# Kernel optimization log

Hardware: AMD Instinct MI355X
Metric: run time of the kernel (lower is better)

Reference implementation:

```python
import jax, jax.numpy as jnp
import numpy as np

B, L, D, P = 2, 2048, 768, 1152
I1, I2 = 2048, 3072
H, HD1, HD2 = 12, 64, 96
NC, NP, ND = 3, 6, 3
EPS, ROPE_BASE = 1e-5, 10000.0
STACK_KEYS = ('wq', 'wk', 'wv', 'wo', 'w1', 'w2', 'w3', 'ln1', 'ln2')


def rope_cache(seq_len, n_elem):
    theta = 1.0 / (ROPE_BASE ** (jnp.arange(0, n_elem, 2, dtype=jnp.float32) / n_elem))
    freqs = jnp.outer(jnp.arange(seq_len, dtype=jnp.float32), theta)
    emb = jnp.concatenate([freqs, freqs], axis=-1)  # [T, n_elem]
    return jnp.cos(emb), jnp.sin(emb)


def apply_rope(x, cos, sin):
    half = x.shape[-1] // 2
    x1, x2 = x[..., :half], x[..., half:]
    return x * cos[None, None] + jnp.concatenate([-x2, x1], axis=-1) * sin[None, None]


def rmsnorm(x, w):
    return x * jax.lax.rsqrt(jnp.mean(x * x, axis=-1, keepdims=True) + EPS) * w


def block(x, p, cos, sin):
    Bx, T, Dm = x.shape
    hd = Dm // H
    h = rmsnorm(x, p['ln1'])
    q = (h @ p['wq']).reshape(Bx, T, H, hd).transpose(0, 2, 1, 3)
    k = (h @ p['wk']).reshape(Bx, T, H, hd).transpose(0, 2, 1, 3)
    v = (h @ p['wv']).reshape(Bx, T, H, hd).transpose(0, 2, 1, 3)
    q, k = apply_rope(q, cos, sin), apply_rope(k, cos, sin)
    scores = jnp.einsum('bhqd,bhkd->bhqk', q, k) / jnp.sqrt(jnp.float32(hd))
    scores = jnp.where(jnp.tril(jnp.ones((T, T), dtype=bool)), scores, -jnp.inf)
    o = jnp.einsum('bhqk,bhkd->bhqd', jax.nn.softmax(scores, axis=-1), v)
    x = x + o.transpose(0, 2, 1, 3).reshape(Bx, T, Dm) @ p['wo']
    h = rmsnorm(x, p['ln2'])
    return x + (jax.nn.silu(h @ p['w1']) * (h @ p['w3'])) @ p['w2']


def stack(x, fl, pre, n_layers, cos, sin):
    for i in range(n_layers):
        p = {k: fl[pre + '_' + k][i] for k in STACK_KEYS}
        x = block(x, p, cos, sin)
    return x


def compressor_trunk(fl, cos, sin):
    h = stack(fl['x'], fl, 'comp', NC, cos, sin)
    h = rmsnorm(h, fl['comp_norm'])
    logits = (jax.nn.silu(h @ fl['router_w1'] + fl['router_b1']) @ fl['router_w2'] + fl['router_b2'])[..., 0]
    probs = jax.nn.sigmoid(logits)
    hard = (probs > 0.5).astype(h.dtype)
    bmask = (probs + jax.lax.stop_gradient(hard - probs)).at[:, 0].set(1.0)  # STE
    return h, bmask


def compute_S(fl):
    cos1, sin1 = rope_cache(fl['x'].shape[1], HD1)
    _, bmask = compressor_trunk(fl, cos1, sin1)
    return int(jnp.max(jnp.sum(bmask, axis=-1)))


def model_forward(fl, S):
    Lx = fl['x'].shape[1]
    cos1, sin1 = rope_cache(Lx, HD1)
    h, bmask = compressor_trunk(fl, cos1, sin1)
    bdet = jax.lax.stop_gradient(bmask)
    counts = jnp.sum(bdet, axis=-1).astype(jnp.int32)  # [B]
    cum = jnp.cumsum(bdet, axis=-1)
    assignment = (cum[:, None, :] == jnp.arange(1, S + 1, dtype=cum.dtype)[None, :, None]).astype(h.dtype)
    select = assignment * bmask[:, None, :]  # [B,S,L] one-hot select, grads via STE
    boundaries = jnp.argsort(1.0 - bdet, axis=-1)[:, :S]  # stable desc sort of 0/1 mask
    xc = jnp.einsum('bsl,bld->bsd', select, h) @ fl['up_w']  # ragged gather as GEMM (as original)
    cos2, sin2 = rope_cache(S, HD2)
    xp = rmsnorm(stack(xc, fl, 'proc', NP, cos2, sin2), fl['proc_norm']) @ fl['down_w']
    # decoder: broadcast each chunk embedding back over its positions
    valid = counts[:, None] > jnp.arange(S)[None, :]
    starts = jnp.where(valid[:, :, None], boundaries[:, :, None], Lx)  # [B,S,1]
    chunk_ids = jnp.sum(jnp.arange(Lx)[None, None, :] >= starts, axis=1) - 1  # [B,L]
    y = jnp.take_along_axis(xp, chunk_ids[..., None], axis=1) + h
    y = stack(y, fl, 'dec', ND, cos1, sin1)
    return rmsnorm(y, fl['dec_norm'])


def setup_inputs():
    ks = iter(jax.random.split(jax.random.key(0), 64))
    def w(*shape):
        return jax.random.normal(next(ks), shape, dtype=jnp.float32) * 0.02
    inp = {'x': jax.random.normal(next(ks), (B, L, D), dtype=jnp.float32)}
    for pre, n, d, it in (('comp', NC, D, I1), ('proc', NP, P, I2), ('dec', ND, D, I1)):
        for nm in ('wq', 'wk', 'wv', 'wo'):
            inp[pre + '_' + nm] = w(n, d, d)
        inp[pre + '_w1'], inp[pre + '_w3'], inp[pre + '_w2'] = w(n, d, it), w(n, d, it), w(n, it, d)
        inp[pre + '_ln1'] = jnp.ones((n, d), jnp.float32)
        inp[pre + '_ln2'] = jnp.ones((n, d), jnp.float32)
        inp[pre + '_norm'] = jnp.ones((d,), jnp.float32)
    inp['router_w1'], inp['router_b1'] = w(D, D), jnp.zeros((D,), jnp.float32)
    inp['router_w2'], inp['router_b2'] = w(D, 1), jnp.zeros((1,), jnp.float32)
    inp['up_w'], inp['down_w'] = w(D, P), w(P, D)
    return inp


def reference(x, comp_wq, comp_wk, comp_wv, comp_wo, comp_w1, comp_w2, comp_w3, comp_ln1, comp_ln2, comp_norm, router_w1, router_b1, router_w2, router_b2, up_w, down_w, proc_wq, proc_wk, proc_wv, proc_wo, proc_w1, proc_w2, proc_w3, proc_ln1, proc_ln2, proc_norm, dec_wq, dec_wk, dec_wv, dec_wo, dec_w1, dec_w2, dec_w3, dec_ln1, dec_ln2, dec_norm):
    fl = dict(locals())  # exactly the forward args
    S = compute_S(fl)  # data-dependent number of chunks (concrete, eager)
    return model_forward(fl, S)
```

## Files before the change

### kernel.cpp

```cpp
#include <hip/hip_runtime.h>
#include <cstdint>

static constexpr int LSEQ = 2048;
static constexpr int NHEAD = 12;

typedef unsigned short u16;
typedef __attribute__((ext_vector_type(8))) short bf16x8;
typedef __attribute__((ext_vector_type(8))) unsigned short u16x8;
typedef __attribute__((ext_vector_type(4))) float f32x4;

#define MFMA16 __builtin_amdgcn_mfma_f32_16x16x32_bf16

union U8cvt { u16 u[8]; bf16x8 v; u16x8 w; };

__device__ __forceinline__ float silu(float a) { return a / (1.f + __expf(-a)); }

__device__ __forceinline__ void splitf(float x, u16& h, u16& l) {
    uint32_t ux = __float_as_uint(x);
    uint32_t uh = (ux + 0x7fffu + ((ux >> 16) & 1u)) >> 16;
    float hf = __uint_as_float(uh << 16);
    float r = x - hf;
    uint32_t ur = __float_as_uint(r);
    uint32_t ul = (ur + 0x7fffu + ((ur >> 16) & 1u)) >> 16;
    h = (u16)uh; l = (u16)ul;
}

__device__ __forceinline__ void gld16(const void* g, void* l) {
    __builtin_amdgcn_global_load_lds((const __attribute__((address_space(1))) void*)g,
                                     (__attribute__((address_space(3))) void*)l, 16, 0, 0);
}

struct SplitEnt { const float* s0; const float* s1; const float* s2;
                  u16* dhi; u16* dlo; int K; int Nper; int nsrc; int bstart; };
struct SplitArgs { SplitEnt e[4]; int ne; };

__global__ __launch_bounds__(256)
void wsplit_k(SplitArgs a)
{
    const int blk = blockIdx.x;
    int ti = a.ne - 1;
    for (int i = 1; i < a.ne; ++i) if (blk < a.e[i].bstart) { ti = i - 1; break; }
    const SplitEnt E = a.e[ti];
    const int N = E.Nper * E.nsrc;
    const int u = (blk - E.bstart) * 256 + threadIdx.x;
    const int n = u % N, kb = u / N;
    const int which = n / E.Nper, col = n - which * E.Nper;
    const float* sp = (which == 0 ? E.s0 : which == 1 ? E.s1 : E.s2)
                      + (size_t)(kb * 8) * E.Nper + col;
    U8cvt hh, ll;
#pragma unroll
    for (int j = 0; j < 8; ++j) splitf(sp[(size_t)j * E.Nper], hh.u[j], ll.u[j]);
    *(u16x8*)(E.dhi + (size_t)u * 8) = hh.w;
    *(u16x8*)(E.dlo + (size_t)u * 8) = ll.w;
}

template<bool MASK>
__global__ __launch_bounds__(256)
void gemm_mfma_k(const u16* __restrict__ Ahi, const u16* __restrict__ Alo,
                 const u16* __restrict__ Bhi, const u16* __restrict__ Blo,
                 const float* __restrict__ Res, float* __restrict__ C,
                 int N, int K, const int* __restrict__ dS)
{
    const int n0 = blockIdx.x * 128;
    const int m0 = blockIdx.y * 128;
    int S = 1 << 30;
    if (MASK) { S = *dS; if ((m0 & (LSEQ - 1)) >= S) return; }

    __shared__ u16 sm[32768];
    u16* sAhi = sm;
    u16* sAlo = sm + 8192;
    u16* sBhi = sm + 16384;
    u16* sBlo = sm + 24576;

    const int t = threadIdx.x;
    const int w = t >> 6, lane = t & 63;
    const int wm = (w >> 1) * 64, wn = (w & 1) * 64;
    const int l15 = lane & 15, l4 = lane >> 4, l7 = lane & 7;

    const f32x4 zf = {0.f, 0.f, 0.f, 0.f};
    f32x4 acc[4][4];
#pragma unroll
    for (int i = 0; i < 4; ++i)
#pragma unroll
        for (int j = 0; j < 4; ++j) acc[i][j] = zf;

    for (int k0 = 0; k0 < K; k0 += 64) {
        __syncthreads();
#pragma unroll
        for (int i = 0; i < 4; ++i) {
            const int q = i * 256 + t;
            const int mrow = q >> 3;
            const int u = (q & 7) ^ (mrow & 7);
            const size_t goff = (size_t)(m0 + mrow) * K + k0 + u * 8;
            const int lbase = i * 2048 + w * 512;
            gld16(Ahi + goff, (void*)(sAhi + lbase));
            gld16(Alo + goff, (void*)(sAlo + lbase));
        }
#pragma unroll
        for (int i = 0; i < 4; ++i) {
            const int q = i * 256 + t;
            const size_t goff = ((size_t)((k0 >> 3) + (q >> 7)) * N + n0 + (q & 127)) * 8;
            const int lbase = i * 2048 + w * 512;
            gld16(Bhi + goff, (void*)(sBhi + lbase));
            gld16(Blo + goff, (void*)(sBlo + lbase));
        }
        __syncthreads();

#pragma unroll
        for (int kk = 0; kk < 2; ++kk) {
            bf16x8 ah[4], al[4], bh[4], bl[4];
#pragma unroll
            for (int mf = 0; mf < 4; ++mf) {
                const int row = wm + mf * 16 + l15;
                const int idx = row * 64 + (((kk * 4 + l4) ^ l7) * 8);
                ah[mf] = *(const bf16x8*)(sAhi + idx);
                al[mf] = *(const bf16x8*)(sAlo + idx);
            }
#pragma unroll
            for (int nf = 0; nf < 4; ++nf) {
                const int idx = ((kk * 4 + l4) * 128 + wn + nf * 16 + l15) * 8;
                bh[nf] = *(const bf16x8*)(sBhi + idx);
                bl[nf] = *(const bf16x8*)(sBlo + idx);
            }
#pragma unroll
            for (int mf = 0; mf < 4; ++mf)
#pragma unroll
                for (int nf = 0; nf < 4; ++nf) {
                    acc[mf][nf] = MFMA16(ah[mf], bh[nf], acc[mf][nf], 0, 0, 0);
                    acc[mf][nf] = MFMA16(ah[mf], bl[nf], acc[mf][nf], 0, 0, 0);
                    acc[mf][nf] = MFMA16(al[mf], bh[nf], acc[mf][nf], 0, 0, 0);
                }
        }
    }

#pragma unroll
    for (int mf = 0; mf < 4; ++mf) {
#pragma unroll
        for (int r = 0; r < 4; ++r) {
            const int gr = m0 + wm + mf * 16 + l4 * 4 + r;
            if (MASK && (gr & (LSEQ - 1)) >= S) continue;
#pragma unroll
            for (int nf = 0; nf < 4; ++nf) {
                const int gc = n0 + wn + nf * 16 + l15;
                float v = acc[mf][nf][r];
                if (Res) v += Res[(size_t)gr * N + gc];
                C[(size_t)gr * N + gc] = v;
            }
        }
    }
}

template<bool F32OUT, bool SPLITOUT>
__global__ __launch_bounds__(256)
void rmsnorm_k(const float* __restrict__ X, const float* __restrict__ w,
               float* __restrict__ OutF, u16* __restrict__ Ohi, u16* __restrict__ Olo,
               int D, const int* __restrict__ dS)
{
    const int row = blockIdx.x;
    if (dS && (row & (LSEQ - 1)) >= *dS) return;
    const float* xr = X + (size_t)row * D;
    float ss = 0.f;
    for (int d = threadIdx.x; d < D; d += 256) { float v = xr[d]; ss += v * v; }
#pragma unroll
    for (int off = 1; off < 64; off <<= 1) ss += __shfl_xor(ss, off);
    __shared__ float red[4];
    if ((threadIdx.x & 63) == 0) red[threadIdx.x >> 6] = ss;
    __syncthreads();
    const float tot = red[0] + red[1] + red[2] + red[3];
    const float rs = rsqrtf(tot / (float)D + 1e-5f);
    for (int d = threadIdx.x; d < D; d += 256) {
        const float y = xr[d] * rs * w[d];
        if (F32OUT) OutF[(size_t)row * D + d] = y;
        if (SPLITOUT) {
            u16 h, l; splitf(y, h, l);
            Ohi[(size_t)row * D + d] = h;
            Olo[(size_t)row * D + d] = l;
        }
    }
}

__global__ __launch_bounds__(256)
void swiglu_k(const float* __restrict__ T13, u16* __restrict__ Shi,
              u16* __restrict__ Slo, int ff, const int* __restrict__ dS)
{
    const int c = blockIdx.x * 256 + threadIdx.x;
    const int cpr = ff >> 3;
    const int row = c / cpr, c8 = c - row * cpr;
    if (row >= 4096) return;
    if (dS && (row & (LSEQ - 1)) >= *dS) return;
    const size_t ba = (size_t)row * (2 * ff) + c8 * 8;
    const float4 a0 = *(const float4*)(T13 + ba);
    const float4 a1 = *(const float4*)(T13 + ba + 4);
    const float4 g0 = *(const float4*)(T13 + ba + ff);
    const float4 g1 = *(const float4*)(T13 + ba + ff + 4);
    float v[8] = { silu(a0.x) * g0.x, silu(a0.y) * g0.y, silu(a0.z) * g0.z, silu(a0.w) * g0.w,
                   silu(a1.x) * g1.x, silu(a1.y) * g1.y, silu(a1.z) * g1.z, silu(a1.w) * g1.w };
    u16 hi[8], lo[8];
#pragma unroll
    for (int j = 0; j < 8; ++j) splitf(v[j], hi[j], lo[j]);
    const size_t bo = (size_t)row * ff + c8 * 8;
    *(u16x8*)(Shi + bo) = *(u16x8*)hi;
    *(u16x8*)(Slo + bo) = *(u16x8*)lo;
}

__global__ void ropetab_k(float* c1, float* s1, float* c2, float* s2)
{
    const int idx = blockIdx.x * 256 + threadIdx.x;
    if (idx < 2048 * 32) {
        const int pos = idx >> 5, i = idx & 31;
        const float th = powf(10000.f, -(float)(2 * i) / 64.f);
        const float v = (float)pos * th;
        c1[idx] = cosf(v); s1[idx] = sinf(v);
    }
    const int idx2 = idx - 2048 * 32;
    if (idx2 >= 0 && idx2 < 2048 * 48) {
        const int pos = idx2 / 48, i = idx2 - (idx2 / 48) * 48;
        const float th = powf(10000.f, -(float)(2 * i) / 96.f);
        const float v = (float)pos * th;
        c2[idx2] = cosf(v); s2[idx2] = sinf(v);
    }
}

template<int HD>
__global__ __launch_bounds__(256)
void prep_k(float* __restrict__ QKV, u16* __restrict__ Khi, u16* __restrict__ Klo,
            u16* __restrict__ Vthi, u16* __restrict__ Vtlo,
            const float* __restrict__ ct, const float* __restrict__ st,
            int dm, const int* __restrict__ dS)
{
    constexpr int half = HD / 2;
    const int s0 = blockIdx.x * 64;
    if (dS && s0 >= *dS) return;
    const int bh = blockIdx.y;
    const int b = bh / NHEAD, h = bh - b * NHEAD;
    const int qstride = 3 * dm;
    const int t = threadIdx.x;

#pragma unroll
    for (int it = 0; it < 64 * half / 256; ++it) {
        const int e = it * 256 + t;
        const int row = e / half, i = e - row * half;
        const int pos = s0 + row;
        const float c = ct[pos * half + i], sn = st[pos * half + i];
        const size_t g = (size_t)(b * LSEQ + pos) * qstride + h * HD + i;
        float x1 = QKV[g], x2 = QKV[g + half];
        QKV[g] = x1 * c - x2 * sn; QKV[g + half] = x2 * c + x1 * sn;
        const size_t gk = g + dm;
        x1 = QKV[gk]; x2 = QKV[gk + half];
        const float k1 = x1 * c - x2 * sn, k2 = x2 * c + x1 * sn;
        const size_t ko = ((size_t)bh * LSEQ + pos) * HD + i;
        u16 hh, ll;
        splitf(k1, hh, ll); Khi[ko] = hh; Klo[ko] = ll;
        splitf(k2, hh, ll); Khi[ko + half] = hh; Klo[ko + half] = ll;
    }

    __shared__ u16 sh[64][HD], sl[64][HD];
    constexpr int C4 = HD / 4;
#pragma unroll
    for (int it = 0; it < 64 * C4 / 256; ++it) {
        const int q = it * 256 + t;
        const int row = q / C4, c4 = q - row * C4;
        const float4 v = *(const float4*)(QKV + (size_t)(b * LSEQ + s0 + row) * qstride
                                          + 2 * dm + h * HD + c4 * 4);
        u16 hh, ll;
        splitf(v.x, hh, ll); sh[row][c4 * 4 + 0] = hh; sl[row][c4 * 4 + 0] = ll;
        splitf(v.y, hh, ll); sh[row][c4 * 4 + 1] = hh; sl[row][c4 * 4 + 1] = ll;
        splitf(v.z, hh, ll); sh[row][c4 * 4 + 2] = hh; sl[row][c4 * 4 + 2] = ll;
        splitf(v.w, hh, ll); sh[row][c4 * 4 + 3] = hh; sl[row][c4 * 4 + 3] = ll;
    }
    __syncthreads();
    const int s8 = t & 7, d0 = t >> 3;
    for (int d = d0; d < HD; d += 32) {
        U8cvt hh, ll;
#pragma unroll
        for (int j = 0; j < 8; ++j) { hh.u[j] = sh[s8 * 8 + j][d]; ll.u[j] = sl[s8 * 8 + j][d]; }
        const size_t vo = ((size_t)bh * HD + d) * LSEQ + s0 + s8 * 8;
        *(u16x8*)(Vthi + vo) = hh.w;
        *(u16x8*)(Vtlo + vo) = ll.w;
    }
}

template<int HD>
__device__ __forceinline__ int kswz(int u, int r) {
    if constexpr (HD == 64) return u ^ (r & 7);
    else return (u & 12) | ((u & 3) ^ (r & 3));
}

template<int HD, int MF>
__global__ __launch_bounds__(256)
void fattn2_k(const float* __restrict__ QKV, const u16* __restrict__ Khi,
              const u16* __restrict__ Klo, const u16* __restrict__ Vthi,
              const u16* __restrict__ Vtlo, u16* __restrict__ Ohi,
              u16* __restrict__ Olo, float* __restrict__ Pacc,
              float* __restrict__ Pml, int dm, float scale,
              const int* __restrict__ dS)
{
    constexpr int BQ = MF * 64;
    constexpr int BK = 64;
    constexpr int KG8 = HD / 8;
    constexpr int KO = HD / 32;
    constexpr int NFP = HD / 16;
    constexpr float NEG = -3.0e38f;

    const int x = blockIdx.x;
    int j, half; bool partial;
    if (x < 32) { j = 16 + (x >> 1); half = x & 1; partial = true; }
    else        { j = x - 32;        half = 0;     partial = false; }
    const int q0 = j * 64;
    int S = 1 << 30;
    if (dS) { S = *dS; if (q0 >= S) return; }
    const int c0 = ((j + 1) >> 1) * 64;
    const int kbeg = (partial && half) ? c0 : 0;
    const int kend = partial ? (half ? (j + 1) * 64 : c0) : (j + 1) * 64;

    const int bh = blockIdx.y;
    const int b = bh / NHEAD, h = bh - b * NHEAD;
    const int qstride = 3 * dm;

    __shared__ u16 smem[2 * BK * HD + 2 * HD * BK + 4 * 2 * MF * 16 * 64];
    u16* sKhi = smem;
    u16* sKlo = sKhi + BK * HD;
    u16* sVhi = sKlo + BK * HD;
    u16* sVlo = sVhi + HD * BK;
    u16* sP   = sVlo + HD * BK;

    const int t = threadIdx.x;
    const int w = t >> 6, lane = t & 63;
    const int l15 = lane & 15, l4 = lane >> 4;
    u16* sPhi = sP + w * (2 * MF * 16 * 64);
    u16* sPlo = sPhi + MF * 16 * 64;

    const int qbase = q0 + w * (MF * 16);

    bf16x8 qh[MF][KO], ql[MF][KO];
#pragma unroll
    for (int mf = 0; mf < MF; ++mf) {
        const float* qp = QKV + (size_t)(b * LSEQ + qbase + mf * 16 + l15) * qstride + h * HD;
#pragma unroll
        for (int ki = 0; ki < KO; ++ki) {
            const float* p = qp + (ki * 4 + l4) * 8;
            U8cvt hh, ll;
#pragma unroll
            for (int jj = 0; jj < 8; ++jj) splitf(p[jj] * scale, hh.u[jj], ll.u[jj]);
            qh[mf][ki] = hh.v; ql[mf][ki] = ll.v;
        }
    }

    float m[MF][4], l[MF][4];
#pragma unroll
    for (int mf = 0; mf < MF; ++mf)
#pragma unroll
        for (int r = 0; r < 4; ++r) { m[mf][r] = NEG; l[mf][r] = 0.f; }
    const f32x4 zf = {0.f, 0.f, 0.f, 0.f};
    f32x4 acc[MF][NFP];
#pragma unroll
    for (int mf = 0; mf < MF; ++mf)
#pragma unroll
        for (int nf = 0; nf < NFP; ++nf) acc[mf][nf] = zf;

    const size_t kbase = (size_t)bh * LSEQ * HD;
    const size_t vbase = (size_t)bh * HD * LSEQ;

    for (int k0 = kbeg; k0 < kend; k0 += BK) {
        __syncthreads();
#pragma unroll
        for (int it = 0; it < BK * KG8 / 256; ++it) {
            const int q = it * 256 + t;
            const int r = q / KG8, u = q - r * KG8;
            const int us = kswz<HD>(u, r);
            const size_t go = kbase + (size_t)(k0 + r) * HD + us * 8;
            gld16(Khi + go, (void*)(sKhi + it * 2048 + w * 512));
            gld16(Klo + go, (void*)(sKlo + it * 2048 + w * 512));
        }
#pragma unroll
        for (int it = 0; it < HD * 8 / 256; ++it) {
            const int q = it * 256 + t;
            const int d = q >> 3, u = q & 7;
            const int us = u ^ (d & 7);
            const size_t go = vbase + (size_t)d * LSEQ + k0 + us * 8;
            gld16(Vthi + go, (void*)(sVhi + it * 2048 + w * 512));
            gld16(Vtlo + go, (void*)(sVlo + it * 2048 + w * 512));
        }
        __syncthreads();

        if (k0 < qbase + MF * 16) {
            f32x4 sc[MF][4];
#pragma unroll
            for (int mf = 0; mf < MF; ++mf)
#pragma unroll
                for (int kf = 0; kf < 4; ++kf) sc[mf][kf] = zf;
            __builtin_amdgcn_s_setprio(1);
#pragma unroll
            for (int kf = 0; kf < 4; ++kf) {
                const int row = kf * 16 + l15;
#pragma unroll
                for (int ki = 0; ki < KO; ++ki) {
                    const int idx = row * HD + kswz<HD>(ki * 4 + l4, row) * 8;
                    const bf16x8 kh = *(const bf16x8*)(sKhi + idx);
                    const bf16x8 kl = *(const bf16x8*)(sKlo + idx);
#pragma unroll
                    for (int mf = 0; mf < MF; ++mf) {
                        sc[mf][kf] = MFMA16(qh[mf][ki], kh, sc[mf][kf], 0, 0, 0);
                        sc[mf][kf] = MFMA16(qh[mf][ki], kl, sc[mf][kf], 0, 0, 0);
                        sc[mf][kf] = MFMA16(ql[mf][ki], kh, sc[mf][kf], 0, 0, 0);
                    }
                }
            }
            __builtin_amdgcn_s_setprio(0);

            if (k0 + 63 > qbase) {
#pragma unroll
                for (int mf = 0; mf < MF; ++mf) {
                    const int qg = qbase + mf * 16 + l4 * 4;
#pragma unroll
                    for (int kf = 0; kf < 4; ++kf) {
                        const int jc = k0 + kf * 16 + l15;
#pragma unroll
                        for (int r = 0; r < 4; ++r)
                            if (jc > qg + r) sc[mf][kf][r] = NEG;
                    }
                }
            }

#pragma unroll
            for (int mf = 0; mf < MF; ++mf) {
                float fac[4];
#pragma unroll
                for (int r = 0; r < 4; ++r) {
                    float mx = fmaxf(fmaxf(sc[mf][0][r], sc[mf][1][r]),
                                     fmaxf(sc[mf][2][r], sc[mf][3][r]));
                    mx = fmaxf(mx, __shfl_xor(mx, 1));
                    mx = fmaxf(mx, __shfl_xor(mx, 2));
                    mx = fmaxf(mx, __shfl_xor(mx, 4));
                    mx = fmaxf(mx, __shfl_xor(mx, 8));
                    const float mn = fmaxf(m[mf][r], mx);
                    fac[r] = __expf(m[mf][r] - mn);
                    float rs = 0.f;
                    float pv[4];
#pragma unroll
                    for (int kf = 0; kf < 4; ++kf) { pv[kf] = __expf(sc[mf][kf][r] - mn); rs += pv[kf]; }
                    rs += __shfl_xor(rs, 1);
                    rs += __shfl_xor(rs, 2);
                    rs += __shfl_xor(rs, 4);
                    rs += __shfl_xor(rs, 8);
                    l[mf][r] = l[mf][r] * fac[r] + rs;
                    m[mf][r] = mn;
                    const int prow = mf * 16 + l4 * 4 + r;
                    const int rx = prow & 7;
#pragma unroll
                    for (int kf = 0; kf < 4; ++kf) {
                        u16 hh, ll; splitf(pv[kf], hh, ll);
                        const int a = prow * 64 + (((kf * 2 + (l15 >> 3)) ^ rx) * 8) + (l15 & 7);
                        sPhi[a] = hh; sPlo[a] = ll;
                    }
                }
#pragma unroll
                for (int nf = 0; nf < NFP; ++nf)
#pragma unroll
                    for (int r = 0; r < 4; ++r) acc[mf][nf][r] *= fac[r];
            }

            bf16x8 ph[MF][2], pl[MF][2];
#pragma unroll
            for (int mf = 0; mf < MF; ++mf)
#pragma unroll
                for (int kk = 0; kk < 2; ++kk) {
                    const int a = (mf * 16 + l15) * 64 + (((kk * 4 + l4) ^ (l15 & 7)) * 8);
                    ph[mf][kk] = *(const bf16x8*)(sPhi + a);
                    pl[mf][kk] = *(const bf16x8*)(sPlo + a);
                }
            __builtin_amdgcn_s_setprio(1);
#pragma unroll
            for (int nf = 0; nf < NFP; ++nf) {
                const int row = nf * 16 + l15;
#pragma unroll
                for (int kk = 0; kk < 2; ++kk) {
                    const int idx = row * 64 + ((kk * 4 + l4) ^ (row & 7)) * 8;
                    const bf16x8 vh = *(const bf16x8*)(sVhi + idx);
                    const bf16x8 vl = *(const bf16x8*)(sVlo + idx);
#pragma unroll
                    for (int mf = 0; mf < MF; ++mf) {
                        acc[mf][nf] = MFMA16(ph[mf][kk], vh, acc[mf][nf], 0, 0, 0);
                        acc[mf][nf] = MFMA16(ph[mf][kk], vl, acc[mf][nf], 0, 0, 0);
                        acc[mf][nf] = MFMA16(pl[mf][kk], vh, acc[mf][nf], 0, 0, 0);
                    }
                }
            }
            __builtin_amdgcn_s_setprio(0);
        }
    }

    if (!partial) {
#pragma unroll
        for (int mf = 0; mf < MF; ++mf)
#pragma unroll
            for (int r = 0; r < 4; ++r) {
                const float rl = 1.f / l[mf][r];
                const size_t ro = (size_t)(b * LSEQ + qbase + mf * 16 + l4 * 4 + r) * dm + h * HD;
#pragma unroll
                for (int nf = 0; nf < NFP; ++nf) {
                    u16 hh, ll; splitf(acc[mf][nf][r] * rl, hh, ll);
                    Ohi[ro + nf * 16 + l15] = hh;
                    Olo[ro + nf * 16 + l15] = ll;
                }
            }
    } else {
        const int pi = (bh * 16 + (j - 16)) * 2 + half;
#pragma unroll
        for (int mf = 0; mf < MF; ++mf)
#pragma unroll
            for (int r = 0; r < 4; ++r) {
                const int row = w * (MF * 16) + mf * 16 + l4 * 4 + r;
                float* pa = Pacc + ((size_t)pi * 64 + row) * HD;
#pragma unroll
                for (int nf = 0; nf < NFP; ++nf)
                    pa[nf * 16 + l15] = acc[mf][nf][r];
                if (l15 == 0) {
                    Pml[((size_t)pi * 64 + row) * 2 + 0] = m[mf][r];
                    Pml[((size_t)pi * 64 + row) * 2 + 1] = l[mf][r];
                }
            }
    }
}

template<int HD>
__global__ __launch_bounds__(256)
void attn_merge_k(const float* __restrict__ Pacc, const float* __restrict__ Pml,
                  u16* __restrict__ Ohi, u16* __restrict__ Olo,
                  int dm, const int* __restrict__ dS)
{
    const int j = 16 + blockIdx.x;
    const int q0 = j * 64;
    if (dS && q0 >= *dS) return;
    const int bh = blockIdx.y;
    const int b = bh / NHEAD, h = bh - b * NHEAD;
    const int pi0 = (bh * 16 + (j - 16)) * 2;
    __shared__ float w0s[64], w1s[64], invs[64];
    const int t = threadIdx.x;
    if (t < 64) {
        const float m0 = Pml[((size_t)pi0 * 64 + t) * 2];
        const float l0 = Pml[((size_t)pi0 * 64 + t) * 2 + 1];
        const float m1 = Pml[((size_t)(pi0 + 1) * 64 + t) * 2];
        const float l1 = Pml[((size_t)(pi0 + 1) * 64 + t) * 2 + 1];
        const float mm = fmaxf(m0, m1);
        const float a = __expf(m0 - mm), c = __expf(m1 - mm);
        w0s[t] = a; w1s[t] = c; invs[t] = 1.f / (a * l0 + c * l1);
    }
    __syncthreads();
    for (int e = t; e < 64 * HD; e += 256) {
        const int row = e / HD, d = e - row * HD;
        const float a0 = Pacc[((size_t)pi0 * 64 + row) * HD + d];
        const float a1 = Pacc[((size_t)(pi0 + 1) * 64 + row) * HD + d];
        const float o = (w0s[row] * a0 + w1s[row] * a1) * invs[row];
        u16 hh, ll; splitf(o, hh, ll);
        const size_t ro = (size_t)(b * LSEQ + q0 + row) * dm + h * HD + d;
        Ohi[ro] = hh; Olo[ro] = ll;
    }
}

__global__ __launch_bounds__(256)
void router2_k(const float* __restrict__ T, const float* __restrict__ b1,
               const float* __restrict__ w2, const float* __restrict__ b2,
               int* __restrict__ mask)
{
    const int row = blockIdx.x;
    const float* tr = T + (size_t)row * 768;
    float p = 0.f;
    for (int d = threadIdx.x; d < 768; d += 256) {
        const float u = tr[d] + b1[d];
        p += u / (1.f + __expf(-u)) * w2[d];
    }
#pragma unroll
    for (int off = 1; off < 64; off <<= 1) p += __shfl_xor(p, off);
    __shared__ float red[4];
    if ((threadIdx.x & 63) == 0) red[threadIdx.x >> 6] = p;
    __syncthreads();
    if (threadIdx.x == 0) {
        const float logit = red[0] + red[1] + red[2] + red[3] + b2[0];
        mask[row] = ((row & (LSEQ - 1)) == 0 || logit > 0.f) ? 1 : 0;
    }
}

__global__ __launch_bounds__(256)
void scan_k(const int* __restrict__ mask, int* __restrict__ cid,
            int* __restrict__ bnd, int* __restrict__ counts)
{
    const int b = blockIdx.x, t = threadIdx.x;
    const int base = b * LSEQ;
    __shared__ int lds[256];
    int loc[8]; int s = 0;
#pragma unroll
    for (int j = 0; j < 8; ++j) { s += mask[base + t * 8 + j]; loc[j] = s; }
    lds[t] = s;
    __syncthreads();
    for (int off = 1; off < 256; off <<= 1) {
        const int v = (t >= off) ? lds[t - off] : 0;
        __syncthreads();
        lds[t] += v;
        __syncthreads();
    }
    const int excl = lds[t] - s;
#pragma unroll
    for (int j = 0; j < 8; ++j) {
        const int e = t * 8 + j;
        const int c = excl + loc[j];
        cid[base + e] = c - 1;
        if (mask[base + e]) bnd[base + c - 1] = e;
    }
    if (t == 255) counts[b] = lds[255];
}

__global__ void smax_k(const int* __restrict__ counts, int* __restrict__ dS)
{
    if (threadIdx.x == 0 && blockIdx.x == 0) {
        int s = counts[0];
        if (counts[1] > s) s = counts[1];
        dS[0] = s;
    }
}

__global__ __launch_bounds__(256)
void gather_k(const float* __restrict__ H, const int* __restrict__ bnd,
              const int* __restrict__ counts, u16* __restrict__ Ghi, u16* __restrict__ Glo)
{
    const int s = blockIdx.x, b = blockIdx.y;
    const int cnt = counts[b];
    const size_t go = ((size_t)b * LSEQ + s) * 768;
    if (s < cnt) {
        const float* h = H + ((size_t)b * LSEQ + bnd[b * LSEQ + s]) * 768;
        for (int d = threadIdx.x; d < 768; d += 256) {
            u16 hi, lo; splitf(h[d], hi, lo);
            Ghi[go + d] = hi; Glo[go + d] = lo;
        }
    } else {
        for (int d = threadIdx.x; d < 768; d += 256) { Ghi[go + d] = 0; Glo[go + d] = 0; }
    }
}

__global__ __launch_bounds__(256)
void ybuild_k(const float* __restrict__ XP, const float* __restrict__ H,
              const int* __restrict__ cid, float* __restrict__ Y)
{
    const int row = blockIdx.x;
    const int b = row >> 11;
    const int c = cid[row];
    const float* xp = XP + ((size_t)b * LSEQ + c) * 768;
    const float* h = H + (size_t)row * 768;
    float* y = Y + (size_t)row * 768;
    for (int d = threadIdx.x; d < 768; d += 256) y[d] = xp[d] + h[d];
}

extern "C" void kernel_launch(void* const* d_in, const int* in_sizes, int n_in,
                              void* d_out, int out_size, void* d_ws, size_t ws_size,
                              hipStream_t stream)
{
    auto F = [&](int i) { return (const float*)d_in[i]; };

    struct SW { const float *wq, *wk, *wv, *wo, *w1, *w3, *w2, *ln1, *ln2, *nrm; };
    SW comp, proc, dec;
    const float *rw1, *rb1, *rw2, *rb2, *upw, *dnw;

    const bool sig = (in_sizes[11] == 589824);
    if (!sig) {
        comp = { F(1), F(2), F(3), F(4), F(5), F(6), F(7), F(8), F(9), F(10) };
        proc = { F(11), F(12), F(13), F(14), F(15), F(16), F(17), F(18), F(19), F(20) };
        dec  = { F(21), F(22), F(23), F(24), F(25), F(26), F(27), F(28), F(29), F(30) };
        rw1 = F(31); rb1 = F(32); rw2 = F(33); rb2 = F(34); upw = F(35); dnw = F(36);
    } else {
        comp = { F(1), F(2), F(3), F(4), F(5), F(7), F(6), F(8), F(9), F(10) };
        rw1 = F(11); rb1 = F(12); rw2 = F(13); rb2 = F(14); upw = F(15); dnw = F(16);
        proc = { F(17), F(18), F(19), F(20), F(21), F(23), F(22), F(24), F(25), F(26) };
        dec  = { F(27), F(28), F(29), F(30), F(31), F(33), F(32), F(34), F(35), F(36) };
    }

    char* ws = (char*)d_ws;
    size_t off = 0;
    auto alloc = [&](size_t bytes) -> void* {
        void* p = ws + off;
        off = (off + bytes + 255) & ~(size_t)255;
        return p;
    };
    float* X    = (float*)alloc(4096ull * 1152 * 4);
    float* BigF = (float*)alloc(4096ull * 6144 * 4);
    float* HC   = (float*)alloc(4096ull * 768 * 4);
    u16* HNhi   = (u16*)alloc(4096ull * 1152 * 2);
    u16* HNlo   = (u16*)alloc(4096ull * 1152 * 2);
    u16* SWhi   = (u16*)alloc(4096ull * 3072 * 2);
    u16* SWlo   = (u16*)alloc(4096ull * 3072 * 2);
    u16* Khi    = (u16*)alloc(24ull * 2048 * 96 * 2);
    u16* Klo    = (u16*)alloc(24ull * 2048 * 96 * 2);
    u16* Vthi   = (u16*)alloc(24ull * 2048 * 96 * 2);
    u16* Vtlo   = (u16*)alloc(24ull * 2048 * 96 * 2);
    float* Pacc = (float*)alloc(24ull * 16 * 2 * 64 * 96 * 4);
    float* Pml  = (float*)alloc(24ull * 16 * 2 * 64 * 2 * 4);
    u16* qkvPhi = (u16*)alloc(3981312ull * 2);
    u16* qkvPlo = (u16*)alloc(3981312ull * 2);
    u16* woPhi  = (u16*)alloc(1327104ull * 2);
    u16* woPlo  = (u16*)alloc(1327104ull * 2);
    u16* w13Phi = (u16*)alloc(7077888ull * 2);
    u16* w13Plo = (u16*)alloc(7077888ull * 2);
    u16* w2Phi  = (u16*)alloc(3538944ull * 2);
    u16* w2Plo  = (u16*)alloc(3538944ull * 2);
    u16* rw1Phi = (u16*)alloc(589824ull * 2);
    u16* rw1Plo = (u16*)alloc(589824ull * 2);
    u16* upwPhi = (u16*)alloc(884736ull * 2);
    u16* upwPlo = (u16*)alloc(884736ull * 2);
    u16* dnwPhi = (u16*)alloc(884736ull * 2);
    u16* dnwPlo = (u16*)alloc(884736ull * 2);
    int* mask   = (int*)alloc(4096 * 4);
    int* cid    = (int*)alloc(4096 * 4);
    int* bnd    = (int*)alloc(4096 * 4);
    int* cnts   = (int*)alloc(2 * 4);
    int* dS     = (int*)alloc(256);
    float* c1   = (float*)alloc(2048ull * 32 * 4);
    float* s1   = (float*)alloc(2048ull * 32 * 4);
    float* c2   = (float*)alloc(2048ull * 48 * 4);
    float* s2   = (float*)alloc(2048ull * 48 * 4);

    float* QKV = BigF;
    float* T13 = BigF;
    float* XP  = BigF;
    u16* Ohi = SWhi;
    u16* Olo = SWlo;

    hipMemcpyAsync(X, F(0), 4096ull * 768 * 4, hipMemcpyDeviceToDevice, stream);
    ropetab_k<<<640, 256, 0, stream>>>(c1, s1, c2, s2);

    {
        SplitArgs sa{};
        sa.ne = 3;
        sa.e[0] = { rw1, nullptr, nullptr, rw1Phi, rw1Plo, 768, 768, 1, 0 };
        sa.e[1] = { upw, nullptr, nullptr, upwPhi, upwPlo, 768, 1152, 1, 288 };
        sa.e[2] = { dnw, nullptr, nullptr, dnwPhi, dnwPlo, 1152, 768, 1, 720 };
        wsplit_k<<<1152, 256, 0, stream>>>(sa);
    }

    auto gemm = [&](const u16* ahi, const u16* alo, const u16* bhi, const u16* blo,
                    const float* res, float* c, int N, int K, const int* ds) {
        if (ds) gemm_mfma_k<true><<<dim3(N / 128, 32), 256, 0, stream>>>(ahi, alo, bhi, blo, res, c, N, K, ds);
        else    gemm_mfma_k<false><<<dim3(N / 128, 32), 256, 0, stream>>>(ahi, alo, bhi, blo, res, c, N, K, nullptr);
    };

    auto run_layer = [&](const SW& W, int li, int dm, int ff, int hd,
                         const float* ct, const float* st, const int* ds) {
        const size_t wsz = (size_t)dm * dm;
        const float* wq = W.wq + (size_t)li * wsz;
        const float* wk = W.wk + (size_t)li * wsz;
        const float* wv = W.wv + (size_t)li * wsz;
        const float* wo = W.wo + (size_t)li * wsz;
        const float* w1 = W.w1 + (size_t)li * dm * ff;
        const float* w3 = W.w3 + (size_t)li * dm * ff;
        const float* w2 = W.w2 + (size_t)li * ff * dm;
        const float* ln1 = W.ln1 + (size_t)li * dm;
        const float* ln2 = W.ln2 + (size_t)li * dm;
        const float scale = 1.0f / sqrtf((float)hd);

        {
            const int b0 = dm * 3 * dm / 2048, b1 = dm * dm / 2048, b2 = dm * 2 * ff / 2048,
                      b3 = ff * dm / 2048;
            SplitArgs sa{};
            sa.ne = 4;
            sa.e[0] = { wq, wk, wv, qkvPhi, qkvPlo, dm, dm, 3, 0 };
            sa.e[1] = { wo, nullptr, nullptr, woPhi, woPlo, dm, dm, 1, b0 };
            sa.e[2] = { w1, w3, nullptr, w13Phi, w13Plo, dm, ff, 2, b0 + b1 };
            sa.e[3] = { w2, nullptr, nullptr, w2Phi, w2Plo, ff, dm, 1, b0 + b1 + b2 };
            wsplit_k<<<b0 + b1 + b2 + b3, 256, 0, stream>>>(sa);
        }

        rmsnorm_k<false, true><<<4096, 256, 0, stream>>>(X, ln1, nullptr, HNhi, HNlo, dm, ds);
        gemm(HNhi, HNlo, qkvPhi, qkvPlo, nullptr, QKV, 3 * dm, dm, ds);
        if (hd == 64) {
            prep_k<64><<<dim3(32, 24), 256, 0, stream>>>(QKV, Khi, Klo, Vthi, Vtlo, ct, st, dm, ds);
            fattn2_k<64, 1><<<dim3(48, 24), 256, 0, stream>>>(QKV, Khi, Klo, Vthi, Vtlo, Ohi, Olo, Pacc, Pml, dm, scale, ds);
            attn_merge_k<64><<<dim3(16, 24), 256, 0, stream>>>(Pacc, Pml, Ohi, Olo, dm, ds);
        } else {
            prep_k<96><<<dim3(32, 24), 256, 0, stream>>>(QKV, Khi, Klo, Vthi, Vtlo, ct, st, dm, ds);
            fattn2_k<96, 1><<<dim3(48, 24), 256, 0, stream>>>(QKV, Khi, Klo, Vthi, Vtlo, Ohi, Olo, Pacc, Pml, dm, scale, ds);
            attn_merge_k<96><<<dim3(16, 24), 256, 0, stream>>>(Pacc, Pml, Ohi, Olo, dm, ds);
        }
        gemm(Ohi, Olo, woPhi, woPlo, X, X, dm, dm, ds);
        rmsnorm_k<false, true><<<4096, 256, 0, stream>>>(X, ln2, nullptr, HNhi, HNlo, dm, ds);
        gemm(HNhi, HNlo, w13Phi, w13Plo, nullptr, T13, 2 * ff, dm, ds);
        swiglu_k<<<(4096 * ff / 8) / 256, 256, 0, stream>>>(T13, SWhi, SWlo, ff, ds);
        gemm(SWhi, SWlo, w2Phi, w2Plo, X, X, dm, ff, ds);
    };

    for (int i = 0; i < 3; ++i) run_layer(comp, i, 768, 2048, 64, c1, s1, nullptr);
    rmsnorm_k<true, true><<<4096, 256, 0, stream>>>(X, comp.nrm, HC, HNhi, HNlo, 768, nullptr);

    gemm(HNhi, HNlo, rw1Phi, rw1Plo, nullptr, T13, 768, 768, nullptr);
    router2_k<<<4096, 256, 0, stream>>>(T13, rb1, rw2, rb2, mask);
    scan_k<<<2, 256, 0, stream>>>(mask, cid, bnd, cnts);
    smax_k<<<1, 64, 0, stream>>>(cnts, dS);

    gather_k<<<dim3(LSEQ, 2), 256, 0, stream>>>(HC, bnd, cnts, HNhi, HNlo);
    gemm(HNhi, HNlo, upwPhi, upwPlo, nullptr, X, 1152, 768, dS);

    for (int i = 0; i < 6; ++i) run_layer(proc, i, 1152, 3072, 96, c2, s2, dS);
    rmsnorm_k<false, true><<<4096, 256, 0, stream>>>(X, proc.nrm, nullptr, HNhi, HNlo, 1152, dS);
    gemm(HNhi, HNlo, dnwPhi, dnwPlo, nullptr, XP, 768, 1152, dS);

    ybuild_k<<<4096, 256, 0, stream>>>(XP, HC, cid, X);
    for (int i = 0; i < 3; ++i) run_layer(dec, i, 768, 2048, 64, c1, s1, nullptr);
    rmsnorm_k<true, false><<<4096, 256, 0, stream>>>(X, dec.nrm, (float*)d_out, nullptr, nullptr, 768, nullptr);
}
```

Before: 5.135 ms.

## Add 256x256 ping-pong MFMA GEMM for QKV and W1/W3 projections

Adds a 512-thread GEMM kernel with 256x256 output tiles, double-buffered LDS staging via global_load_lds, split barrier phases and s_setprio to interleave MFMA with LDS reads and prefetch. It is used for the wide QKV and fused W1/W3 projections. For dm=1152 the QKV output width is padded to 3584 (a multiple of 256) with zero columns produced by the weight-split kernel, and the attention kernels take an explicit row stride. The larger tiles raise arithmetic intensity per block but give fewer blocks (occupancy and tail risk), and the padding adds some wasted work.

Measured after the change: 5.695 ms. +10.9%, slower.

```diff
diff --git a/kernel.cpp b/kernel.cpp
--- a/kernel.cpp
+++ b/kernel.cpp
@@ -30,8 +30,11 @@
                                      (__attribute__((address_space(3))) void*)l, 16, 0, 0);
 }
 
+#define BARRIER() do { asm volatile("" ::: "memory"); \
+    __builtin_amdgcn_s_barrier(); asm volatile("" ::: "memory"); } while (0)
+
 struct SplitEnt { const float* s0; const float* s1; const float* s2;
-                  u16* dhi; u16* dlo; int K; int Nper; int nsrc; int bstart; };
+                  u16* dhi; u16* dlo; int K; int Nper; int nsrc; int bstart; int Ntot; };
 struct SplitArgs { SplitEnt e[4]; int ne; };
 
 __global__ __launch_bounds__(256)
@@ -41,15 +44,21 @@
     int ti = a.ne - 1;
     for (int i = 1; i < a.ne; ++i) if (blk < a.e[i].bstart) { ti = i - 1; break; }
     const SplitEnt E = a.e[ti];
-    const int N = E.Nper * E.nsrc;
+    const int N = E.Ntot;
     const int u = (blk - E.bstart) * 256 + threadIdx.x;
     const int n = u % N, kb = u / N;
-    const int which = n / E.Nper, col = n - which * E.Nper;
-    const float* sp = (which == 0 ? E.s0 : which == 1 ? E.s1 : E.s2)
-                      + (size_t)(kb * 8) * E.Nper + col;
+    const int which = n / E.Nper;
     U8cvt hh, ll;
-#pragma unroll
-    for (int j = 0; j < 8; ++j) splitf(sp[(size_t)j * E.Nper], hh.u[j], ll.u[j]);
+    if (which >= E.nsrc) {
+#pragma unroll
+        for (int j = 0; j < 8; ++j) { hh.u[j] = 0; ll.u[j] = 0; }
+    } else {
+        const int col = n - which * E.Nper;
+        const float* sp = (which == 0 ? E.s0 : which == 1 ? E.s1 : E.s2)
+                          + (size_t)(kb * 8) * E.Nper + col;
+#pragma unroll
+        for (int j = 0; j < 8; ++j) splitf(sp[(size_t)j * E.Nper], hh.u[j], ll.u[j]);
+    }
     *(u16x8*)(E.dhi + (size_t)u * 8) = hh.w;
     *(u16x8*)(E.dlo + (size_t)u * 8) = ll.w;
 }
@@ -142,6 +151,171 @@
 #pragma unroll
             for (int nf = 0; nf < 4; ++nf) {
                 const int gc = n0 + wn + nf * 16 + l15;
+                float v = acc[mf][nf][r];
+                if (Res) v += Res[(size_t)gr * N + gc];
+                C[(size_t)gr * N + gc] = v;
+            }
+        }
+    }
+}
+
+template<bool MASK>
+__global__ __launch_bounds__(512, 2)
+void gemm256_k(const u16* __restrict__ Ahi, const u16* __restrict__ Alo,
+               const u16* __restrict__ Bhi, const u16* __restrict__ Blo,
+               const float* __restrict__ Res, float* __restrict__ C,
+               int N, int K, const int* __restrict__ dS)
+{
+    const int n0 = blockIdx.x * 256;
+    const int m0 = blockIdx.y * 256;
+    int S = 1 << 30;
+    if (MASK) { S = *dS; if ((m0 & (LSEQ - 1)) >= S) return; }
+
+    __shared__ u16 sm[65536];
+
+    const int tid = threadIdx.x;
+    const int w = tid >> 6, lane = tid & 63;
+    const int wm = w >> 2, wn = w & 3;
+    const int l15 = lane & 15, l4 = lane >> 4;
+
+    const int srow = tid >> 3;
+    const int ssl  = (tid & 7) ^ (srow & 7);
+    const u16* aPtr = (ssl < 4 ? Ahi : Alo);
+    const u16* bPtr = (ssl < 4 ? Bhi : Blo);
+    const size_t aBase = (size_t)(m0 + srow) * K + (ssl & 3) * 8;
+    const size_t bBase = ((size_t)(ssl & 3) * N + n0 + srow) * 8;
+    const int ldst = w * 512;
+
+    const f32x4 zf = {0.f, 0.f, 0.f, 0.f};
+    f32x4 acc[8][4];
+#pragma unroll
+    for (int i = 0; i < 8; ++i)
+#pragma unroll
+        for (int j = 0; j < 4; ++j) acc[i][j] = zf;
+
+    auto stageA4 = [&](int k0, u16* dA) {
+#pragma unroll
+        for (int u = 0; u < 4; ++u)
+            gld16(aPtr + aBase + k0 + (size_t)(u * 64) * K, (void*)(dA + u * 4096 + ldst));
+    };
+    auto stageB4 = [&](int kb0, u16* dB) {
+#pragma unroll
+        for (int u = 0; u < 4; ++u)
+            gld16(bPtr + bBase + (size_t)kb0 * N * 8 + u * 512, (void*)(dB + u * 4096 + ldst));
+    };
+    auto rdT = [&](const u16* s, int r0, int ishi) -> bf16x8 {
+        const int row = r0 + l15;
+        const int sl = (l4 + (ishi ? 0 : 4)) ^ (row & 7);
+        return *(const bf16x8*)(s + row * 64 + sl * 8);
+    };
+
+    const int NT = K >> 5;
+    stageA4(0, sm);            stageB4(0, sm + 16384);
+    stageA4(32, sm + 32768);   stageB4(4, sm + 49152);
+    asm volatile("s_waitcnt vmcnt(8)" ::: "memory");
+    BARRIER();
+
+    for (int t = 0; t < NT; ++t) {
+        u16* sA = sm + (t & 1) * 32768;
+        u16* sB = sA + 16384;
+        const bool pf = (t + 2 < NT);
+
+        bf16x8 a0h[4], a0l[4], a1h[4], a1l[4], b0h[2], b0l[2], b1h[2], b1l[2];
+
+#pragma unroll
+        for (int i = 0; i < 4; ++i) {
+            a0h[i] = rdT(sA, wm * 128 + i * 16, 1);
+            a0l[i] = rdT(sA, wm * 128 + i * 16, 0);
+        }
+#pragma unroll
+        for (int j = 0; j < 2; ++j) {
+            b0h[j] = rdT(sB, wn * 64 + j * 16, 1);
+            b0l[j] = rdT(sB, wn * 64 + j * 16, 0);
+        }
+        BARRIER();
+        __builtin_amdgcn_s_setprio(1);
+#pragma unroll
+        for (int i = 0; i < 4; ++i)
+#pragma unroll
+            for (int j = 0; j < 2; ++j) {
+                acc[i][j] = MFMA16(a0h[i], b0h[j], acc[i][j], 0, 0, 0);
+                acc[i][j] = MFMA16(a0h[i], b0l[j], acc[i][j], 0, 0, 0);
+                acc[i][j] = MFMA16(a0l[i], b0h[j], acc[i][j], 0, 0, 0);
+            }
+        __builtin_amdgcn_s_setprio(0);
+        asm volatile("s_waitcnt lgkmcnt(0)" ::: "memory");
+        BARRIER();
+
+#pragma unroll
+        for (int j = 0; j < 2; ++j) {
+            b1h[j] = rdT(sB, wn * 64 + 32 + j * 16, 1);
+            b1l[j] = rdT(sB, wn * 64 + 32 + j * 16, 0);
+        }
+        BARRIER();
+        __builtin_amdgcn_s_setprio(1);
+#pragma unroll
+        for (int i = 0; i < 4; ++i)
+#pragma unroll
+            for (int j = 0; j < 2; ++j) {
+                acc[i][2 + j] = MFMA16(a0h[i], b1h[j], acc[i][2 + j], 0, 0, 0);
+                acc[i][2 + j] = MFMA16(a0h[i], b1l[j], acc[i][2 + j], 0, 0, 0);
+                acc[i][2 + j] = MFMA16(a0l[i], b1h[j], acc[i][2 + j], 0, 0, 0);
+            }
+        __builtin_amdgcn_s_setprio(0);
+        asm volatile("s_waitcnt lgkmcnt(0)" ::: "memory");
+        BARRIER();
+
+#pragma unroll
+        for (int i = 0; i < 4; ++i) {
+            a1h[i] = rdT(sA, wm * 128 + 64 + i * 16, 1);
+            a1l[i] = rdT(sA, wm * 128 + 64 + i * 16, 0);
+        }
+        if (pf) stageB4((t + 2) * 4, sB);
+        BARRIER();
+        __builtin_amdgcn_s_setprio(1);
+#pragma unroll
+        for (int i = 0; i < 4; ++i)
+#pragma unroll
+            for (int j = 0; j < 2; ++j) {
+                acc[4 + i][2 + j] = MFMA16(a1h[i], b1h[j], acc[4 + i][2 + j], 0, 0, 0);
+                acc[4 + i][2 + j] = MFMA16(a1h[i], b1l[j], acc[4 + i][2 + j], 0, 0, 0);
+                acc[4 + i][2 + j] = MFMA16(a1l[i], b1h[j], acc[4 + i][2 + j], 0, 0, 0);
+            }
+        __builtin_amdgcn_s_setprio(0);
+        asm volatile("s_waitcnt lgkmcnt(0)" ::: "memory");
+        BARRIER();
+
+        if (pf) stageA4((t + 2) * 32, sA);
+        BARRIER();
+        __builtin_amdgcn_s_setprio(1);
+#pragma unroll
+        for (int i = 0; i < 4; ++i)
+#pragma unroll
+            for (int j = 0; j < 2; ++j) {
+                acc[4 + i][j] = MFMA16(a1h[i], b0h[j], acc[4 + i][j], 0, 0, 0);
+                acc[4 + i][j] = MFMA16(a1h[i], b0l[j], acc[4 + i][j], 0, 0, 0);
+                acc[4 + i][j] = MFMA16(a1l[i], b0h[j], acc[4 + i][j], 0, 0, 0);
+            }
+        __builtin_amdgcn_s_setprio(0);
+
+        if (t + 1 < NT) {
+            if (pf) { asm volatile("s_waitcnt vmcnt(8)" ::: "memory"); }
+            else    { asm volatile("s_waitcnt vmcnt(0)" ::: "memory"); }
+            BARRIER();
+        }
+    }
+
+    const int gr0 = m0 + wm * 128;
+    const int gc0 = n0 + wn * 64;
+#pragma unroll
+    for (int mf = 0; mf < 8; ++mf) {
+#pragma unroll
+        for (int r = 0; r < 4; ++r) {
+            const int gr = gr0 + mf * 16 + l4 * 4 + r;
+            if (MASK && (gr & (LSEQ - 1)) >= S) continue;
+#pragma unroll
+            for (int nf = 0; nf < 4; ++nf) {
+                const int gc = gc0 + nf * 16 + l15;
                 float v = acc[mf][nf][r];
                 if (Res) v += Res[(size_t)gr * N + gc];
                 C[(size_t)gr * N + gc] = v;
@@ -226,14 +400,14 @@
 void prep_k(float* __restrict__ QKV, u16* __restrict__ Khi, u16* __restrict__ Klo,
             u16* __restrict__ Vthi, u16* __restrict__ Vtlo,
             const float* __restrict__ ct, const float* __restrict__ st,
-            int dm, const int* __restrict__ dS)
+            int dm, int qs, const int* __restrict__ dS)
 {
     constexpr int half = HD / 2;
     const int s0 = blockIdx.x * 64;
     if (dS && s0 >= *dS) return;
     const int bh = blockIdx.y;
     const int b = bh / NHEAD, h = bh - b * NHEAD;
-    const int qstride = 3 * dm;
+    const int qstride = qs;
     const int t = threadIdx.x;
 
 #pragma unroll
@@ -292,7 +466,7 @@
               const u16* __restrict__ Klo, const u16* __restrict__ Vthi,
               const u16* __restrict__ Vtlo, u16* __restrict__ Ohi,
               u16* __restrict__ Olo, float* __restrict__ Pacc,
-              float* __restrict__ Pml, int dm, float scale,
+              float* __restrict__ Pml, int dm, int qs, float scale,
               const int* __restrict__ dS)
 {
     constexpr int BQ = MF * 64;
@@ -315,7 +489,7 @@
 
     const int bh = blockIdx.y;
     const int b = bh / NHEAD, h = bh - b * NHEAD;
-    const int qstride = 3 * dm;
+    const int qstride = qs;
 
     __shared__ u16 smem[2 * BK * HD + 2 * HD * BK + 4 * 2 * MF * 16 * 64];
     u16* sKhi = smem;
@@ -693,8 +867,8 @@
     u16* Vtlo   = (u16*)alloc(24ull * 2048 * 96 * 2);
     float* Pacc = (float*)alloc(24ull * 16 * 2 * 64 * 96 * 4);
     float* Pml  = (float*)alloc(24ull * 16 * 2 * 64 * 2 * 4);
-    u16* qkvPhi = (u16*)alloc(3981312ull * 2);
-    u16* qkvPlo = (u16*)alloc(3981312ull * 2);
+    u16* qkvPhi = (u16*)alloc(4128768ull * 2);
+    u16* qkvPlo = (u16*)alloc(4128768ull * 2);
     u16* woPhi  = (u16*)alloc(1327104ull * 2);
     u16* woPlo  = (u16*)alloc(1327104ull * 2);
     u16* w13Phi = (u16*)alloc(7077888ull * 2);
@@ -729,9 +903,9 @@
     {
         SplitArgs sa{};
         sa.ne = 3;
-        sa.e[0] = { rw1, nullptr, nullptr, rw1Phi, rw1Plo, 768, 768, 1, 0 };
-        sa.e[1] = { upw, nullptr, nullptr, upwPhi, upwPlo, 768, 1152, 1, 288 };
-        sa.e[2] = { dnw, nullptr, nullptr, dnwPhi, dnwPlo, 1152, 768, 1, 720 };
+        sa.e[0] = { rw1, nullptr, nullptr, rw1Phi, rw1Plo, 768, 768, 1, 0, 768 };
+        sa.e[1] = { upw, nullptr, nullptr, upwPhi, upwPlo, 768, 1152, 1, 288, 1152 };
+        sa.e[2] = { dnw, nullptr, nullptr, dnwPhi, dnwPlo, 1152, 768, 1, 720, 768 };
         wsplit_k<<<1152, 256, 0, stream>>>(sa);
     }
 
@@ -739,6 +913,11 @@
                     const float* res, float* c, int N, int K, const int* ds) {
         if (ds) gemm_mfma_k<true><<<dim3(N / 128, 32), 256, 0, stream>>>(ahi, alo, bhi, blo, res, c, N, K, ds);
         else    gemm_mfma_k<false><<<dim3(N / 128, 32), 256, 0, stream>>>(ahi, alo, bhi, blo, res, c, N, K, nullptr);
+    };
+    auto gemm256 = [&](const u16* ahi, const u16* alo, const u16* bhi, const u16* blo,
+                       const float* res, float* c, int N, int K, const int* ds) {
+        if (ds) gemm256_k<true><<<dim3(N / 256, 16), 512, 0, stream>>>(ahi, alo, bhi, blo, res, c, N, K, ds);
+        else    gemm256_k<false><<<dim3(N / 256, 16), 512, 0, stream>>>(ahi, alo, bhi, blo, res, c, N, K, nullptr);
     };
 
     auto run_layer = [&](const SW& W, int li, int dm, int ff, int hd,
@@ -754,33 +933,34 @@
         const float* ln1 = W.ln1 + (size_t)li * dm;
         const float* ln2 = W.ln2 + (size_t)li * dm;
         const float scale = 1.0f / sqrtf((float)hd);
+        const int NQ = (dm == 1152) ? 3584 : 3 * dm;
 
         {
-            const int b0 = dm * 3 * dm / 2048, b1 = dm * dm / 2048, b2 = dm * 2 * ff / 2048,
+            const int b0 = dm * NQ / 2048, b1 = dm * dm / 2048, b2 = dm * 2 * ff / 2048,
                       b3 = ff * dm / 2048;
             SplitArgs sa{};
             sa.ne = 4;
-            sa.e[0] = { wq, wk, wv, qkvPhi, qkvPlo, dm, dm, 3, 0 };
-            sa.e[1] = { wo, nullptr, nullptr, woPhi, woPlo, dm, dm, 1, b0 };
-            sa.e[2] = { w1, w3, nullptr, w13Phi, w13Plo, dm, ff, 2, b0 + b1 };
-            sa.e[3] = { w2, nullptr, nullptr, w2Phi, w2Plo, ff, dm, 1, b0 + b1 + b2 };
+            sa.e[0] = { wq, wk, wv, qkvPhi, qkvPlo, dm, dm, 3, 0, NQ };
+            sa.e[1] = { wo, nullptr, nullptr, woPhi, woPlo, dm, dm, 1, b0, dm };
+            sa.e[2] = { w1, w3, nullptr, w13Phi, w13Plo, dm, ff, 2, b0 + b1, 2 * ff };
+            sa.e[3] = { w2, nullptr, nullptr, w2Phi, w2Plo, ff, dm, 1, b0 + b1 + b2, dm };
             wsplit_k<<<b0 + b1 + b2 + b3, 256, 0, stream>>>(sa);
         }
 
         rmsnorm_k<false, true><<<4096, 256, 0, stream>>>(X, ln1, nullptr, HNhi, HNlo, dm, ds);
-        gemm(HNhi, HNlo, qkvPhi, qkvPlo, nullptr, QKV, 3 * dm, dm, ds);
+        gemm256(HNhi, HNlo, qkvPhi, qkvPlo, nullptr, QKV, NQ, dm, ds);
         if (hd == 64) {
-            prep_k<64><<<dim3(32, 24), 256, 0, stream>>>(QKV, Khi, Klo, Vthi, Vtlo, ct, st, dm, ds);
-            fattn2_k<64, 1><<<dim3(48, 24), 256, 0, stream>>>(QKV, Khi, Klo, Vthi, Vtlo, Ohi, Olo, Pacc, Pml, dm, scale, ds);
+            prep_k<64><<<dim3(32, 24), 256, 0, stream>>>(QKV, Khi, Klo, Vthi, Vtlo, ct, st, dm, NQ, ds);
+            fattn2_k<64, 1><<<dim3(48, 24), 256, 0, stream>>>(QKV, Khi, Klo, Vthi, Vtlo, Ohi, Olo, Pacc, Pml, dm, NQ, scale, ds);
             attn_merge_k<64><<<dim3(16, 24), 256, 0, stream>>>(Pacc, Pml, Ohi, Olo, dm, ds);
         } else {
-            prep_k<96><<<dim3(32, 24), 256, 0, stream>>>(QKV, Khi, Klo, Vthi, Vtlo, ct, st, dm, ds);
-            fattn2_k<96, 1><<<dim3(48, 24), 256, 0, stream>>>(QKV, Khi, Klo, Vthi, Vtlo, Ohi, Olo, Pacc, Pml, dm, scale, ds);
+            prep_k<96><<<dim3(32, 24), 256, 0, stream>>>(QKV, Khi, Klo, Vthi, Vtlo, ct, st, dm, NQ, ds);
+            fattn2_k<96, 1><<<dim3(48, 24), 256, 0, stream>>>(QKV, Khi, Klo, Vthi, Vtlo, Ohi, Olo, Pacc, Pml, dm, NQ, scale, ds);
             attn_merge_k<96><<<dim3(16, 24), 256, 0, stream>>>(Pacc, Pml, Ohi, Olo, dm, ds);
         }
         gemm(Ohi, Olo, woPhi, woPlo, X, X, dm, dm, ds);
         rmsnorm_k<false, true><<<4096, 256, 0, stream>>>(X, ln2, nullptr, HNhi, HNlo, dm, ds);
-        gemm(HNhi, HNlo, w13Phi, w13Plo, nullptr, T13, 2 * ff, dm, ds);
+        gemm256(HNhi, HNlo, w13Phi, w13Plo, nullptr, T13, 2 * ff, dm, ds);
         swiglu_k<<<(4096 * ff / 8) / 256, 256, 0, stream>>>(T13, SWhi, SWlo, ff, ds);
         gemm(SWhi, SWlo, w2Phi, w2Plo, X, X, dm, ff, ds);
     };
```

## Register-prefetch next K/V tile during attention compute in flash attention kernel

Applied to the files above, without the earlier changes.

Replaces the load-then-compute loop in the flash attention kernel with a software pipeline. The first K/V tile is loaded into LDS before the loop. Each iteration then issues global loads for the next tile into registers, computes on the current tile, and stores the prefetched registers to LDS between two barriers. This hides global memory latency behind the MFMA work, at the cost of extra VGPR pressure (hi and lo K/V tiles held in registers) that may lower occupancy.

Result: slower. 5.250 ms (+2.2%).

```diff
diff --git a/kernel.cpp b/kernel.cpp
--- a/kernel.cpp
+++ b/kernel.cpp
@@ -295,11 +295,12 @@
               float* __restrict__ Pml, int dm, float scale,
               const int* __restrict__ dS)
 {
-    constexpr int BQ = MF * 64;
     constexpr int BK = 64;
     constexpr int KG8 = HD / 8;
     constexpr int KO = HD / 32;
     constexpr int NFP = HD / 16;
+    constexpr int KI = BK * KG8 / 256;
+    constexpr int VI = HD * 8 / 256;
     constexpr float NEG = -3.0e38f;
 
     const int x = blockIdx.x;
@@ -332,6 +333,23 @@
 
     const int qbase = q0 + w * (MF * 16);
 
+    const size_t kbase = (size_t)bh * LSEQ * HD;
+    const size_t vbase = (size_t)bh * HD * LSEQ;
+
+    size_t kgo[KI], vgo[VI];
+#pragma unroll
+    for (int it = 0; it < KI; ++it) {
+        const int q = it * 256 + t;
+        const int r = q / KG8, u = q - r * KG8;
+        kgo[it] = kbase + (size_t)r * HD + kswz<HD>(u, r) * 8;
+    }
+#pragma unroll
+    for (int it = 0; it < VI; ++it) {
+        const int q = it * 256 + t;
+        const int d = q >> 3, u = q & 7;
+        vgo[it] = vbase + (size_t)d * LSEQ + (u ^ (d & 7)) * 8;
+    }
+
     bf16x8 qh[MF][KO], ql[MF][KO];
 #pragma unroll
     for (int mf = 0; mf < MF; ++mf) {
@@ -358,30 +376,38 @@
 #pragma unroll
         for (int nf = 0; nf < NFP; ++nf) acc[mf][nf] = zf;
 
-    const size_t kbase = (size_t)bh * LSEQ * HD;
-    const size_t vbase = (size_t)bh * HD * LSEQ;
+#pragma unroll
+    for (int it = 0; it < KI; ++it) {
+        const size_t go = kgo[it] + (size_t)kbeg * HD;
+        gld16(Khi + go, (void*)(sKhi + (it * 256 + t) * 8));
+        gld16(Klo + go, (void*)(sKlo + (it * 256 + t) * 8));
+    }
+#pragma unroll
+    for (int it = 0; it < VI; ++it) {
+        const size_t go = vgo[it] + kbeg;
+        gld16(Vthi + go, (void*)(sVhi + (it * 256 + t) * 8));
+        gld16(Vtlo + go, (void*)(sVlo + (it * 256 + t) * 8));
+    }
+    __syncthreads();
 
     for (int k0 = kbeg; k0 < kend; k0 += BK) {
-        __syncthreads();
-#pragma unroll
-        for (int it = 0; it < BK * KG8 / 256; ++it) {
-            const int q = it * 256 + t;
-            const int r = q / KG8, u = q - r * KG8;
-            const int us = kswz<HD>(u, r);
-            const size_t go = kbase + (size_t)(k0 + r) * HD + us * 8;
-            gld16(Khi + go, (void*)(sKhi + it * 2048 + w * 512));
-            gld16(Klo + go, (void*)(sKlo + it * 2048 + w * 512));
-        }
-#pragma unroll
-        for (int it = 0; it < HD * 8 / 256; ++it) {
-            const int q = it * 256 + t;
-            const int d = q >> 3, u = q & 7;
-            const int us = u ^ (d & 7);
-            const size_t go = vbase + (size_t)d * LSEQ + k0 + us * 8;
-            gld16(Vthi + go, (void*)(sVhi + it * 2048 + w * 512));
-            gld16(Vtlo + go, (void*)(sVlo + it * 2048 + w * 512));
-        }
-        __syncthreads();
+        const bool nx = (k0 + BK < kend);
+        u16x8 nkh[KI], nkl[KI], nvh[VI], nvl[VI];
+        if (nx) {
+            const int kn = k0 + BK;
+#pragma unroll
+            for (int it = 0; it < KI; ++it) {
+                const size_t go = kgo[it] + (size_t)kn * HD;
+                nkh[it] = *(const u16x8*)(Khi + go);
+                nkl[it] = *(const u16x8*)(Klo + go);
+            }
+#pragma unroll
+            for (int it = 0; it < VI; ++it) {
+                const size_t go = vgo[it] + kn;
+                nvh[it] = *(const u16x8*)(Vthi + go);
+                nvl[it] = *(const u16x8*)(Vtlo + go);
+            }
+        }
 
         if (k0 < qbase + MF * 16) {
             f32x4 sc[MF][4];
@@ -488,6 +514,21 @@
             }
             __builtin_amdgcn_s_setprio(0);
         }
+
+        __syncthreads();
+        if (nx) {
+#pragma unroll
+            for (int it = 0; it < KI; ++it) {
+                *(u16x8*)(sKhi + (it * 256 + t) * 8) = nkh[it];
+                *(u16x8*)(sKlo + (it * 256 + t) * 8) = nkl[it];
+            }
+#pragma unroll
+            for (int it = 0; it < VI; ++it) {
+                *(u16x8*)(sVhi + (it * 256 + t) * 8) = nvh[it];
+                *(u16x8*)(sVlo + (it * 256 + t) * 8) = nvl[it];
+            }
+        }
+        __syncthreads();
     }
 
     if (!partial) {
```
